# Optimization experiments

Hardware: AMD Instinct MI355X
Metric: run time of the kernel (lower is better)

## Reference

```python
import jax, jax.numpy as jnp
import numpy as np

B, S, D, H = 1, 4096, 1024, 16
HD = D // H  # head_dim = 64


def setup_inputs() -> dict:
    key = jax.random.key(0)
    k1, k2, k3 = jax.random.split(key, 3)
    scale = 0.02
    return {
        "x": jax.random.normal(k1, (B, S, D), dtype=jnp.float32),
        "w_qkv": jax.random.normal(k2, (D, 3 * D), dtype=jnp.float32) * scale,
        "b_qkv": jnp.zeros((3 * D,), dtype=jnp.float32),
        "w_proj": jax.random.normal(k3, (D, D), dtype=jnp.float32) * scale,
        "b_proj": jnp.zeros((D,), dtype=jnp.float32),
    }


def reference(x, w_qkv, b_qkv, w_proj, b_proj):
    b, s, d = x.shape
    qkv = x @ w_qkv + b_qkv                      # [b, s, 3d]
    q, k, v = jnp.split(qkv, 3, axis=-1)
    # [b, h, s, hd]
    q = q.reshape(b, s, H, HD).transpose(0, 2, 1, 3)
    k = k.reshape(b, s, H, HD).transpose(0, 2, 1, 3)
    v = v.reshape(b, s, H, HD).transpose(0, 2, 1, 3)
    score = jnp.einsum("bhqd,bhkd->bhqk", q, k) / jnp.sqrt(jnp.float32(HD))
    causal = jnp.tril(jnp.ones((s, s), dtype=bool))
    score = jnp.where(causal, score, -jnp.inf)
    attn = jax.nn.softmax(score, axis=-1)        # dropout omitted (eval mode, p effectively 0)
    out = jnp.einsum("bhqk,bhkd->bhqd", attn, v)  # [b, h, s, hd]
    out = out.transpose(0, 2, 1, 3).reshape(b, s, d)
    return out @ w_proj + b_proj
```

## Files before the change

### kernel.cpp

```cpp
#include <hip/hip_runtime.h>
#include <hip/hip_bf16.h>
#include <math.h>

typedef __bf16 bf16;
typedef __bf16 bf16x8 __attribute__((ext_vector_type(8)));
typedef __bf16 bf16x4 __attribute__((ext_vector_type(4)));
typedef float f32x4 __attribute__((ext_vector_type(4)));

#define S_ 4096
#define D_ 1024
#define H_ 16
#define HD_ 64
#define N3_ 3072
#define NSPLIT 4

typedef const __attribute__((address_space(1))) void* gas1_t;
typedef __attribute__((address_space(3))) void* las3_t;
static __device__ __forceinline__ void g2l16(const void* g, void* l) {
  __builtin_amdgcn_global_load_lds((gas1_t)g, (las3_t)l, 16, 0, 0);
}

__global__ __launch_bounds__(256) void prep_kernel(const float* __restrict__ x,
                                                   bf16* __restrict__ xb,
                                                   const float* __restrict__ w_qkv,
                                                   bf16* __restrict__ wqkvT,
                                                   const float* __restrict__ w_proj,
                                                   bf16* __restrict__ wprojT) {
  __shared__ float t[32][33];
  const int b = blockIdx.x;
  if (b < 4096) {
    int i = (b * 256 + threadIdx.x) * 4;
    float4 v = *(const float4*)(x + i);
    bf16x4 o;
    o.x = (bf16)v.x; o.y = (bf16)v.y; o.z = (bf16)v.z; o.w = (bf16)v.w;
    *(bf16x4*)(xb + i) = o;
    return;
  }
  const float* in; bf16* outp; int ldin, bx, by;
  if (b < 7168) { int b2 = b - 4096; in = w_qkv;  outp = wqkvT;  ldin = N3_; bx = (b2 % 96) * 32; by = (b2 / 96) * 32; }
  else          { int b3 = b - 7168; in = w_proj; outp = wprojT; ldin = D_;  bx = (b3 % 32) * 32; by = (b3 / 32) * 32; }
  const int tx = threadIdx.x & 31, ty = threadIdx.x >> 5;
#pragma unroll
  for (int i = 0; i < 4; ++i)
    t[ty + i * 8][tx] = in[(size_t)(by + ty + i * 8) * ldin + bx + tx];
  __syncthreads();
#pragma unroll
  for (int i = 0; i < 4; ++i)
    outp[(size_t)(bx + ty + i * 8) * D_ + by + tx] = (bf16)t[tx][ty + i * 8];
}

template <int BN>
__global__ __launch_bounds__(256) void gemm_bt(const bf16* __restrict__ A,
                                               const bf16* __restrict__ Bt,
                                               const float* __restrict__ bias,
                                               bf16* __restrict__ outb,
                                               float* __restrict__ outf,
                                               bf16* __restrict__ vTout,
                                               int M, int N, int K,
                                               int qlim, float qscale) {
  constexpr int NT = BN / 32;
  __shared__ bf16 sA[128 * 32];
  __shared__ bf16 sB[BN * 32];
  const int tid = threadIdx.x;
  const int wave = tid >> 6, lane = tid & 63;
  const int col = lane & 15, quad = lane >> 4;
  const int wm = (wave & 1) * 64, wn = (wave >> 1) * (BN / 2);
  const long bm = (long)blockIdx.x * 128, bn = (long)blockIdx.y * BN;
  const int srow = tid >> 2;
  const int soff = (tid & 3) * 8;

  f32x4 acc[4][NT] = {};

  for (int kb = 0; kb < K; kb += 32) {
    __syncthreads();
    g2l16(A + (bm + srow) * (long)K + kb + soff,      &sA[tid * 8]);
    g2l16(A + (bm + 64 + srow) * (long)K + kb + soff, &sA[2048 + tid * 8]);
#pragma unroll
    for (int i = 0; i < BN / 64; ++i)
      g2l16(Bt + (bn + i * 64 + srow) * (long)K + kb + soff, &sB[i * 2048 + tid * 8]);
    __syncthreads();

    bf16x8 af[4], bfr[NT];
#pragma unroll
    for (int t = 0; t < 4; ++t)
      af[t] = *(const bf16x8*)(&sA[(wm + t * 16 + col) * 32 + quad * 8]);
#pragma unroll
    for (int t = 0; t < NT; ++t)
      bfr[t] = *(const bf16x8*)(&sB[(wn + t * 16 + col) * 32 + quad * 8]);
#pragma unroll
    for (int mt = 0; mt < 4; ++mt)
#pragma unroll
      for (int nt = 0; nt < NT; ++nt)
        acc[mt][nt] = __builtin_amdgcn_mfma_f32_16x16x32_bf16(af[mt], bfr[nt], acc[mt][nt], 0, 0, 0);
  }

#pragma unroll
  for (int mt = 0; mt < 4; ++mt) {
#pragma unroll
    for (int nt = 0; nt < NT; ++nt) {
      long gn = bn + wn + nt * 16 + col;
      float bv = bias ? bias[gn] : 0.f;
      if (vTout && gn >= 2 * D_) {
        bf16x4 vv;
        long gm0 = bm + wm + mt * 16 + quad * 4;
#pragma unroll
        for (int i = 0; i < 4; ++i) vv[i] = (bf16)(acc[mt][nt][i] + bv);
        *(bf16x4*)(&vTout[(gn - 2 * D_) * (long)S_ + gm0]) = vv;
      } else {
        float sc = (gn < qlim) ? qscale : 1.0f;
#pragma unroll
        for (int i = 0; i < 4; ++i) {
          long gm = bm + wm + mt * 16 + quad * 4 + i;
          float v = (acc[mt][nt][i] + bv) * sc;
          if (outf) outf[gm * N + gn] = v;
          else      outb[gm * N + gn] = (bf16)v;
        }
      }
    }
  }
}

__device__ __forceinline__ int swz_g(int row) {
  return (row & 3) | ((((row >> 2) ^ (row >> 3)) & 1) << 2);
}

__global__ __launch_bounds__(256) void attn_kernel(const bf16* __restrict__ qkv,
                                                   const bf16* __restrict__ vT,
                                                   bf16* __restrict__ Opart,
                                                   float* __restrict__ lws) {
  __shared__ bf16 sK[2][64 * 64];
  __shared__ bf16 sV[2][64 * 64];
  const int hh = blockIdx.x;
  const int qb = (int)(gridDim.y - 1 - blockIdx.y);
  const int sp = blockIdx.z;
  const int tid = threadIdx.x;
  const int wave = tid >> 6, lane = tid & 63;
  const int col = lane & 15, quad = lane >> 4;
  const int qbase = qb * 128 + wave * 32;

  const bf16* qp0 = qkv + (size_t)(qbase + col) * N3_ + hh * HD_;
  bf16x8 aq[2][2];
  aq[0][0] = *(const bf16x8*)(qp0 + quad * 8);
  aq[0][1] = *(const bf16x8*)(qp0 + 32 + quad * 8);
  aq[1][0] = *(const bf16x8*)(qp0 + 16 * N3_ + quad * 8);
  aq[1][1] = *(const bf16x8*)(qp0 + 16 * N3_ + 32 + quad * 8);

  bf16x8 ones;
#pragma unroll
  for (int j = 0; j < 8; ++j) ones[j] = (bf16)1.0f;

  f32x4 acc[2][4] = {};
  f32x4 acc_l[2] = {};

  const bf16* kgbase = qkv + D_ + hh * HD_;
  const bf16* vgbase = vT + (size_t)hh * HD_ * S_;
  const int krow = (col >> 2) * 8 + (col & 3);
  const int niter = 2 * (qb + 1);
  const int base = niter >> 2, rem = niter & 3;
  const int it0 = sp * base + (sp < rem ? sp : rem);
  const int len = base + (sp < rem ? 1 : 0);
  const int it1 = it0 + len;

  const int lrow = lane >> 3, sl = lane & 7;
  const int row0 = wave * 8 + lrow;
  const int row1 = row0 + 32;
  const int c0 = sl ^ swz_g(row0);
  const int c1 = sl ^ swz_g(row1);
  const int dst0 = wave * 512 + lane * 8;
  const int dst1 = dst0 + 2048;

  if (len > 0) {
    {
      const int kb0 = it0 * 64;
      g2l16(kgbase + (size_t)(kb0 + row0) * N3_ + c0 * 8, &sK[0][dst0]);
      g2l16(kgbase + (size_t)(kb0 + row1) * N3_ + c1 * 8, &sK[0][dst1]);
      g2l16(vgbase + (size_t)row0 * S_ + kb0 + c0 * 8, &sV[0][dst0]);
      g2l16(vgbase + (size_t)row1 * S_ + kb0 + c1 * 8, &sV[0][dst1]);
    }
    __syncthreads();

    for (int j = it0; j < it1; ++j) {
      const int kb = j * 64;
      const int cur = (j - it0) & 1;
      if (j + 1 < it1) {
        const int kb2 = kb + 64;
        const int nb = cur ^ 1;
        g2l16(kgbase + (size_t)(kb2 + row0) * N3_ + c0 * 8, &sK[nb][dst0]);
        g2l16(kgbase + (size_t)(kb2 + row1) * N3_ + c1 * 8, &sK[nb][dst1]);
        g2l16(vgbase + (size_t)row0 * S_ + kb2 + c0 * 8, &sV[nb][dst0]);
        g2l16(vgbase + (size_t)row1 * S_ + kb2 + c1 * 8, &sV[nb][dst1]);
      }

      if (kb < qbase + 32) {
        const bool act0 = kb < qbase + 16;
        const bf16* kc = &sK[cur][0];
        const bf16* vc = &sV[cur][0];

        f32x4 st[2][4];
        __builtin_amdgcn_s_setprio(1);
#pragma unroll
        for (int t = 0; t < 4; ++t) {
          int row = (t >> 1) * 32 + (t & 1) * 4 + krow;
          int pc = quad ^ swz_g(row);
          bf16x8 bk0 = *(const bf16x8*)(kc + row * 64 + pc * 8);
          bf16x8 bk1 = *(const bf16x8*)(kc + row * 64 + (pc ^ 4) * 8);
          if (act0) {
            f32x4 z = {};
            z = __builtin_amdgcn_mfma_f32_16x16x32_bf16(bk0, aq[0][0], z, 0, 0, 0);
            st[0][t] = __builtin_amdgcn_mfma_f32_16x16x32_bf16(bk1, aq[0][1], z, 0, 0, 0);
          }
          f32x4 z = {};
          z = __builtin_amdgcn_mfma_f32_16x16x32_bf16(bk0, aq[1][0], z, 0, 0, 0);
          st[1][t] = __builtin_amdgcn_mfma_f32_16x16x32_bf16(bk1, aq[1][1], z, 0, 0, 0);
        }
        __builtin_amdgcn_s_setprio(0);

        bf16x8 pfrag[2][2];
#pragma unroll
        for (int s2 = 0; s2 < 2; ++s2) {
          if (s2 == 0 && !act0) continue;
          const int rowbase = qbase + 16 * s2;
          float p[4][4];
          if (kb + 63 <= rowbase) {
#pragma unroll
            for (int t = 0; t < 4; ++t)
#pragma unroll
              for (int r = 0; r < 4; ++r)
                p[t][r] = __builtin_amdgcn_exp2f(st[s2][t][r]);
          } else {
#pragma unroll
            for (int t = 0; t < 4; ++t)
#pragma unroll
              for (int r = 0; r < 4; ++r) {
                int key = kb + (t >> 1) * 32 + quad * 8 + (t & 1) * 4 + r;
                p[t][r] = (key > rowbase + col)
                              ? 0.f
                              : __builtin_amdgcn_exp2f(st[s2][t][r]);
              }
          }
#pragma unroll
          for (int c = 0; c < 2; ++c)
#pragma unroll
            for (int j2 = 0; j2 < 4; ++j2) {
              pfrag[s2][c][j2]     = (bf16)p[2 * c][j2];
              pfrag[s2][c][j2 + 4] = (bf16)p[2 * c + 1][j2];
            }
        }

        __builtin_amdgcn_s_setprio(1);
#pragma unroll
        for (int c = 0; c < 2; ++c) {
#pragma unroll
          for (int n = 0; n < 4; ++n) {
            int row = n * 16 + col;
            int pc = (4 * c + quad) ^ swz_g(row);
            bf16x8 bv = *(const bf16x8*)(vc + row * 64 + pc * 8);
            if (act0)
              acc[0][n] = __builtin_amdgcn_mfma_f32_16x16x32_bf16(pfrag[0][c], bv, acc[0][n], 0, 0, 0);
            acc[1][n] = __builtin_amdgcn_mfma_f32_16x16x32_bf16(pfrag[1][c], bv, acc[1][n], 0, 0, 0);
          }
          if (act0)
            acc_l[0] = __builtin_amdgcn_mfma_f32_16x16x32_bf16(pfrag[0][c], ones, acc_l[0], 0, 0, 0);
          acc_l[1] = __builtin_amdgcn_mfma_f32_16x16x32_bf16(pfrag[1][c], ones, acc_l[1], 0, 0, 0);
        }
        __builtin_amdgcn_s_setprio(0);
      }

      __syncthreads();
    }
  }

  bf16* Op = Opart + (size_t)sp * S_ * D_;
#pragma unroll
  for (int s2 = 0; s2 < 2; ++s2) {
    const int rowbase = qbase + 16 * s2;
    if (col == 0) {
#pragma unroll
      for (int r = 0; r < 4; ++r)
        lws[((size_t)sp * H_ + hh) * S_ + rowbase + quad * 4 + r] = acc_l[s2][r];
    }
#pragma unroll
    for (int n = 0; n < 4; ++n)
#pragma unroll
      for (int r = 0; r < 4; ++r)
        Op[(size_t)(rowbase + quad * 4 + r) * D_ + hh * HD_ + n * 16 + col] =
            (bf16)acc[s2][n][r];
  }
}

__global__ __launch_bounds__(256) void attn_combine(const bf16* __restrict__ Opart,
                                                    const float* __restrict__ lws,
                                                    bf16* __restrict__ outb) {
  int e = (blockIdx.x * 256 + threadIdx.x) * 8;
  int s = e >> 10;
  int h = (e & (D_ - 1)) >> 6;
  float l = 0.f;
#pragma unroll
  for (int sp = 0; sp < NSPLIT; ++sp) l += lws[((size_t)sp * H_ + h) * S_ + s];
  float inv = 1.0f / l;
  float o[8] = {};
#pragma unroll
  for (int sp = 0; sp < NSPLIT; ++sp) {
    bf16x8 a = *(const bf16x8*)(Opart + (size_t)sp * S_ * D_ + e);
#pragma unroll
    for (int j = 0; j < 8; ++j) o[j] += (float)a[j];
  }
  bf16x8 r;
#pragma unroll
  for (int j = 0; j < 8; ++j) r[j] = (bf16)(o[j] * inv);
  *(bf16x8*)(outb + e) = r;
}

extern "C" void kernel_launch(void* const* d_in, const int* in_sizes, int n_in,
                              void* d_out, int out_size, void* d_ws, size_t ws_size,
                              hipStream_t stream) {
  const float* x      = (const float*)d_in[0];
  const float* w_qkv  = (const float*)d_in[1];
  const float* b_qkv  = (const float*)d_in[2];
  const float* w_proj = (const float*)d_in[3];
  const float* b_proj = (const float*)d_in[4];
  float* out = (float*)d_out;

  bf16* xb     = (bf16*)d_ws;
  bf16* wqkvT  = xb + (size_t)S_ * D_;
  bf16* wprojT = wqkvT + (size_t)N3_ * D_;
  bf16* qkv    = wprojT + (size_t)D_ * D_;
  bf16* vT     = qkv + (size_t)S_ * N3_;
  bf16* Opart  = vT + (size_t)D_ * S_;
  float* lws   = (float*)(Opart + (size_t)NSPLIT * S_ * D_);
  bf16* attn   = xb;

  const float QSCALE = 0.125f * 1.44269504088896f;

  prep_kernel<<<dim3(8192), 256, 0, stream>>>(x, xb, w_qkv, wqkvT, w_proj, wprojT);
  gemm_bt<128><<<dim3(S_ / 128, N3_ / 128), 256, 0, stream>>>(
      xb, wqkvT, b_qkv, qkv, nullptr, vT, S_, N3_, D_, D_, QSCALE);
  attn_kernel<<<dim3(H_, S_ / 128, NSPLIT), 256, 0, stream>>>(qkv, vT, Opart, lws);
  attn_combine<<<dim3((S_ * D_) / 2048), 256, 0, stream>>>(Opart, lws, attn);
  gemm_bt<64><<<dim3(S_ / 128, D_ / 64), 256, 0, stream>>>(
      attn, wprojT, b_proj, nullptr, out, nullptr, S_, D_, D_, 0, 1.0f);
}
```

Measured before the change: 214.3 us.

## Load K/V fragments directly from global memory instead of staging through LDS

Removes the double-buffered shared-memory staging of K and V tiles, along with the block-wide barriers. Each wave now loads its MFMA operands directly from global memory, relying on cache. The loop range is also capped per wave so waves skip fully masked key blocks instead of idling at barriers. In exchange, the four waves no longer share K/V data, so global and L2 traffic per block rises, and the act0 skip of the first 16-row subtile is dropped.

```diff
diff --git a/kernel.cpp b/kernel.cpp
--- a/kernel.cpp
+++ b/kernel.cpp
@@ -120,16 +120,10 @@
   }
 }
 
-__device__ __forceinline__ int swz_g(int row) {
-  return (row & 3) | ((((row >> 2) ^ (row >> 3)) & 1) << 2);
-}
-
 __global__ __launch_bounds__(256) void attn_kernel(const bf16* __restrict__ qkv,
                                                    const bf16* __restrict__ vT,
                                                    bf16* __restrict__ Opart,
                                                    float* __restrict__ lws) {
-  __shared__ bf16 sK[2][64 * 64];
-  __shared__ bf16 sV[2][64 * 64];
   const int hh = blockIdx.x;
   const int qb = (int)(gridDim.y - 1 - blockIdx.y);
   const int sp = blockIdx.z;
@@ -155,118 +149,81 @@
   const bf16* kgbase = qkv + D_ + hh * HD_;
   const bf16* vgbase = vT + (size_t)hh * HD_ * S_;
   const int krow = (col >> 2) * 8 + (col & 3);
+
+  const bf16* kp[4];
+#pragma unroll
+  for (int t = 0; t < 4; ++t)
+    kp[t] = kgbase + (size_t)((t >> 1) * 32 + (t & 1) * 4 + krow) * N3_ + quad * 8;
+  const bf16* vp[4];
+#pragma unroll
+  for (int n = 0; n < 4; ++n)
+    vp[n] = vgbase + (size_t)(n * 16 + col) * S_ + quad * 8;
+
   const int niter = 2 * (qb + 1);
   const int base = niter >> 2, rem = niter & 3;
   const int it0 = sp * base + (sp < rem ? sp : rem);
-  const int len = base + (sp < rem ? 1 : 0);
-  const int it1 = it0 + len;
-
-  const int lrow = lane >> 3, sl = lane & 7;
-  const int row0 = wave * 8 + lrow;
-  const int row1 = row0 + 32;
-  const int c0 = sl ^ swz_g(row0);
-  const int c1 = sl ^ swz_g(row1);
-  const int dst0 = wave * 512 + lane * 8;
-  const int dst1 = dst0 + 2048;
-
-  if (len > 0) {
-    {
-      const int kb0 = it0 * 64;
-      g2l16(kgbase + (size_t)(kb0 + row0) * N3_ + c0 * 8, &sK[0][dst0]);
-      g2l16(kgbase + (size_t)(kb0 + row1) * N3_ + c1 * 8, &sK[0][dst1]);
-      g2l16(vgbase + (size_t)row0 * S_ + kb0 + c0 * 8, &sV[0][dst0]);
-      g2l16(vgbase + (size_t)row1 * S_ + kb0 + c1 * 8, &sV[0][dst1]);
-    }
-    __syncthreads();
-
-    for (int j = it0; j < it1; ++j) {
-      const int kb = j * 64;
-      const int cur = (j - it0) & 1;
-      if (j + 1 < it1) {
-        const int kb2 = kb + 64;
-        const int nb = cur ^ 1;
-        g2l16(kgbase + (size_t)(kb2 + row0) * N3_ + c0 * 8, &sK[nb][dst0]);
-        g2l16(kgbase + (size_t)(kb2 + row1) * N3_ + c1 * 8, &sK[nb][dst1]);
-        g2l16(vgbase + (size_t)row0 * S_ + kb2 + c0 * 8, &sV[nb][dst0]);
-        g2l16(vgbase + (size_t)row1 * S_ + kb2 + c1 * 8, &sV[nb][dst1]);
+  int it1 = it0 + base + (sp < rem ? 1 : 0);
+  const int jcap = (qbase + 32 + 63) >> 6;
+  if (it1 > jcap) it1 = jcap;
+
+  for (int j = it0; j < it1; ++j) {
+    const int kb = j * 64;
+    const size_t ko = (size_t)kb * N3_;
+
+    f32x4 st[2][4];
+#pragma unroll
+    for (int t = 0; t < 4; ++t) {
+      bf16x8 bk0 = *(const bf16x8*)(kp[t] + ko);
+      bf16x8 bk1 = *(const bf16x8*)(kp[t] + ko + 32);
+      f32x4 z0 = {};
+      z0 = __builtin_amdgcn_mfma_f32_16x16x32_bf16(bk0, aq[0][0], z0, 0, 0, 0);
+      st[0][t] = __builtin_amdgcn_mfma_f32_16x16x32_bf16(bk1, aq[0][1], z0, 0, 0, 0);
+      f32x4 z1 = {};
+      z1 = __builtin_amdgcn_mfma_f32_16x16x32_bf16(bk0, aq[1][0], z1, 0, 0, 0);
+      st[1][t] = __builtin_amdgcn_mfma_f32_16x16x32_bf16(bk1, aq[1][1], z1, 0, 0, 0);
+    }
+
+    bf16x8 pfrag[2][2];
+#pragma unroll
+    for (int s2 = 0; s2 < 2; ++s2) {
+      const int rowbase = qbase + 16 * s2;
+      float p[4][4];
+      if (kb + 63 <= rowbase) {
+#pragma unroll
+        for (int t = 0; t < 4; ++t)
+#pragma unroll
+          for (int r = 0; r < 4; ++r)
+            p[t][r] = __builtin_amdgcn_exp2f(st[s2][t][r]);
+      } else {
+#pragma unroll
+        for (int t = 0; t < 4; ++t)
+#pragma unroll
+          for (int r = 0; r < 4; ++r) {
+            int key = kb + (t >> 1) * 32 + quad * 8 + (t & 1) * 4 + r;
+            p[t][r] = (key > rowbase + col)
+                          ? 0.f
+                          : __builtin_amdgcn_exp2f(st[s2][t][r]);
+          }
       }
-
-      if (kb < qbase + 32) {
-        const bool act0 = kb < qbase + 16;
-        const bf16* kc = &sK[cur][0];
-        const bf16* vc = &sV[cur][0];
-
-        f32x4 st[2][4];
-        __builtin_amdgcn_s_setprio(1);
-#pragma unroll
-        for (int t = 0; t < 4; ++t) {
-          int row = (t >> 1) * 32 + (t & 1) * 4 + krow;
-          int pc = quad ^ swz_g(row);
-          bf16x8 bk0 = *(const bf16x8*)(kc + row * 64 + pc * 8);
-          bf16x8 bk1 = *(const bf16x8*)(kc + row * 64 + (pc ^ 4) * 8);
-          if (act0) {
-            f32x4 z = {};
-            z = __builtin_amdgcn_mfma_f32_16x16x32_bf16(bk0, aq[0][0], z, 0, 0, 0);
-            st[0][t] = __builtin_amdgcn_mfma_f32_16x16x32_bf16(bk1, aq[0][1], z, 0, 0, 0);
-          }
-          f32x4 z = {};
-          z = __builtin_amdgcn_mfma_f32_16x16x32_bf16(bk0, aq[1][0], z, 0, 0, 0);
-          st[1][t] = __builtin_amdgcn_mfma_f32_16x16x32_bf16(bk1, aq[1][1], z, 0, 0, 0);
+#pragma unroll
+      for (int c = 0; c < 2; ++c)
+#pragma unroll
+        for (int j2 = 0; j2 < 4; ++j2) {
+          pfrag[s2][c][j2]     = (bf16)p[2 * c][j2];
+          pfrag[s2][c][j2 + 4] = (bf16)p[2 * c + 1][j2];
         }
-        __builtin_amdgcn_s_setprio(0);
-
-        bf16x8 pfrag[2][2];
-#pragma unroll
-        for (int s2 = 0; s2 < 2; ++s2) {
-          if (s2 == 0 && !act0) continue;
-          const int rowbase = qbase + 16 * s2;
-          float p[4][4];
-          if (kb + 63 <= rowbase) {
-#pragma unroll
-            for (int t = 0; t < 4; ++t)
-#pragma unroll
-              for (int r = 0; r < 4; ++r)
-                p[t][r] = __builtin_amdgcn_exp2f(st[s2][t][r]);
-          } else {
-#pragma unroll
-            for (int t = 0; t < 4; ++t)
-#pragma unroll
-              for (int r = 0; r < 4; ++r) {
-                int key = kb + (t >> 1) * 32 + quad * 8 + (t & 1) * 4 + r;
-                p[t][r] = (key > rowbase + col)
-                              ? 0.f
-                              : __builtin_amdgcn_exp2f(st[s2][t][r]);
-              }
-          }
-#pragma unroll
-          for (int c = 0; c < 2; ++c)
-#pragma unroll
-            for (int j2 = 0; j2 < 4; ++j2) {
-              pfrag[s2][c][j2]     = (bf16)p[2 * c][j2];
-              pfrag[s2][c][j2 + 4] = (bf16)p[2 * c + 1][j2];
-            }
-        }
-
-        __builtin_amdgcn_s_setprio(1);
-#pragma unroll
-        for (int c = 0; c < 2; ++c) {
-#pragma unroll
-          for (int n = 0; n < 4; ++n) {
-            int row = n * 16 + col;
-            int pc = (4 * c + quad) ^ swz_g(row);
-            bf16x8 bv = *(const bf16x8*)(vc + row * 64 + pc * 8);
-            if (act0)
-              acc[0][n] = __builtin_amdgcn_mfma_f32_16x16x32_bf16(pfrag[0][c], bv, acc[0][n], 0, 0, 0);
-            acc[1][n] = __builtin_amdgcn_mfma_f32_16x16x32_bf16(pfrag[1][c], bv, acc[1][n], 0, 0, 0);
-          }
-          if (act0)
-            acc_l[0] = __builtin_amdgcn_mfma_f32_16x16x32_bf16(pfrag[0][c], ones, acc_l[0], 0, 0, 0);
-          acc_l[1] = __builtin_amdgcn_mfma_f32_16x16x32_bf16(pfrag[1][c], ones, acc_l[1], 0, 0, 0);
-        }
-        __builtin_amdgcn_s_setprio(0);
+    }
+
+#pragma unroll
+    for (int c = 0; c < 2; ++c) {
+#pragma unroll
+      for (int n = 0; n < 4; ++n) {
+        bf16x8 bv = *(const bf16x8*)(vp[n] + kb + c * 32);
+        acc[0][n] = __builtin_amdgcn_mfma_f32_16x16x32_bf16(pfrag[0][c], bv, acc[0][n], 0, 0, 0);
+        acc[1][n] = __builtin_amdgcn_mfma_f32_16x16x32_bf16(pfrag[1][c], bv, acc[1][n], 0, 0, 0);
       }
-
-      __syncthreads();
+      acc_l[0] = __builtin_amdgcn_mfma_f32_16x16x32_bf16(pfrag[0][c], ones, acc_l[0], 0, 0, 0);
+      acc_l[1] = __builtin_amdgcn_mfma_f32_16x16x32_bf16(pfrag[1][c], ones, acc_l[1], 0, 0, 0);
     }
   }
 
```

New measurement: 302.7 us. 41.3% more time.
